# Performance work log

Measured on AMD Instinct MI355X. Metric: run time of the kernel, lower is better.

The kernel has to match this reference:

```python
import jax, jax.numpy as jnp
import numpy as np

N = 4096            # reservoir size
MAX_DIM = 4608      # max_dynamic_reservoir_dim
INPUT_DIM = 1024
LEAK_RATE = 0.1
SPIKE_THRESHOLD = 0.5
T, B = 128, 128


def setup_inputs() -> dict:
    key = jax.random.key(0)
    k1, k2, k3, k4 = jax.random.split(key, 4)
    x = jax.random.normal(k1, (T, B, INPUT_DIM), dtype=jnp.float32)
    state0 = jnp.zeros((B, MAX_DIM), dtype=jnp.float32)
    # keras RandomNormal default stddev=0.05 for reservoir, 0.1 for input/gate
    W_res = 0.05 * jax.random.normal(k2, (N, N), dtype=jnp.float32)
    W_in = 0.1 * jax.random.normal(k3, (N, INPUT_DIM), dtype=jnp.float32)
    W_gate = 0.1 * jax.random.normal(k4, (3 * N, INPUT_DIM), dtype=jnp.float32)
    return {"x": x, "state0": state0, "W_res": W_res, "W_in": W_in, "W_gate": W_gate}


def _cell(prev_padded, x_t, W_res, W_in, W_gate):
    prev = prev_padded[:, :N]                                  # [B, N]
    input_part = x_t @ W_in.T                                  # [B, N]
    reservoir_part = prev @ W_res                              # [B, N]
    gate = jax.nn.sigmoid(x_t @ W_gate.T)                      # [B, 3N]
    i_gate, f_gate, o_gate = jnp.split(gate, 3, axis=-1)
    state = (1.0 - LEAK_RATE) * (f_gate * prev) \
            + LEAK_RATE * jnp.tanh(i_gate * (input_part + reservoir_part))
    state = o_gate * state
    state = jnp.where(state > SPIKE_THRESHOLD, state - SPIKE_THRESHOLD, state)
    padded = jnp.concatenate(
        [state, jnp.zeros((state.shape[0], MAX_DIM - N), dtype=state.dtype)], axis=1)
    return padded


def reference(x, state0, W_res, W_in, W_gate):
    def step(carry, x_t):
        new = _cell(carry, x_t, W_res, W_in, W_gate)
        return new, new
    _, outs = jax.lax.scan(step, state0, x)   # outs: [T, B, MAX_DIM]
    return outs
```

## Files before the change

### kernel.cpp

```cpp
#include <hip/hip_runtime.h>
#include <hip/hip_bf16.h>
#include <hip/hip_fp16.h>

#define N_RES   4096
#define MAXD    4608
#define IN_DIM  1024
#define T_STEPS 128
#define B_SZ    128

typedef __attribute__((ext_vector_type(8))) short bf16x8;
typedef __attribute__((ext_vector_type(8))) _Float16 f16x8;
typedef __attribute__((ext_vector_type(4))) float f32x4;

__device__ __forceinline__ short f2bf(float x) {
  union { float f; unsigned u; } v; v.f = x;
  unsigned r = v.u + 0x7fffu + ((v.u >> 16) & 1u);
  return (short)(r >> 16);
}
__device__ __forceinline__ short f2h(float x) {
  union { _Float16 h; short s; } u; u.h = (_Float16)x; return u.s;
}
__device__ __forceinline__ float h2f(short s) {
  union { _Float16 h; short s; } u; u.s = s; return (float)u.h;
}

__device__ __forceinline__ void gload16(const void* g, void* l) {
  __builtin_amdgcn_global_load_lds(
      (const __attribute__((address_space(1))) void*)g,
      (__attribute__((address_space(3))) void*)l,
      16, 0, 0);
}

__global__ void k_zero_pad(float* __restrict__ out) {
  int row = blockIdx.x;
  int t = threadIdx.x;
  *(float4*)(out + (size_t)row * MAXD + N_RES + t * 4) = float4{0.f, 0.f, 0.f, 0.f};
}

__global__ void k_init_state(const float* __restrict__ s0,
                             float* __restrict__ sF, short* __restrict__ sB) {
  int i = blockIdx.x * 256 + threadIdx.x;
  int m = i >> 12, n = i & 4095;
  float v = s0[m * MAXD + n];
  sF[i] = v;
  sB[i] = f2bf(v);
}

__global__ void k_wres_t(const float* __restrict__ W, short* __restrict__ bt) {
  __shared__ float tile[64][65];
  int k0 = blockIdx.y * 64, n0 = blockIdx.x * 64;
  int tx = threadIdx.x & 63, ty = threadIdx.x >> 6;
  #pragma unroll
  for (int r = 0; r < 64; r += 4)
    tile[r + ty][tx] = W[(long)(k0 + r + ty) * N_RES + n0 + tx];
  __syncthreads();
  #pragma unroll
  for (int r = 0; r < 64; r += 4)
    bt[(long)(n0 + r + ty) * N_RES + k0 + tx] = f2bf(tile[tx][r + ty]);
}

__global__ void k_build_b2(const float* __restrict__ Win,
                           const float* __restrict__ Wg, short* __restrict__ B2) {
  int r = blockIdx.x;
  const float* src = (r < N_RES) ? (Win + (long)r * IN_DIM)
                                 : (Wg + (long)(r - N_RES) * IN_DIM);
  short* dst = B2 + (long)r * IN_DIM;
  for (int c = threadIdx.x; c < IN_DIM; c += 256)
    dst[c] = f2h(src[c]);
}

__global__ void k_build_a2(const float* __restrict__ x, short* __restrict__ A2, int t0) {
  int r = blockIdx.x;
  const float* src = x + (long)(t0 * B_SZ + r) * IN_DIM;
  short* dst = A2 + (long)r * IN_DIM;
  for (int c = threadIdx.x; c < IN_DIM; c += 256)
    dst[c] = f2h(src[c]);
}

__global__ __launch_bounds__(512, 2) void k_gemm_pre(
    const short* __restrict__ A2, const short* __restrict__ B2,
    _Float16* __restrict__ ip, _Float16* __restrict__ gates, int Mrows) {
  __shared__ short lA[2][2][128 * 64];
  __shared__ short lB[2][2][128 * 64];
  int tid = threadIdx.x, lane = tid & 63, wid = tid >> 6;
  int wr = wid >> 2, wc = wid & 3;

  int nwg = gridDim.x, orig = blockIdx.x;
  int mtiles = nwg >> 6;
  int mt, nt;
  if ((mtiles & 3) == 0) {
    int xcd = orig & 7, idx = orig >> 3;
    int w = idx & 31, sq = idx >> 5;
    nt = xcd * 8 + (w & 7);
    mt = sq * 4 + (w >> 3);
  } else {
    int qx = nwg >> 3, rx = nwg & 7, xcd = orig & 7;
    int wgid = (xcd < rx ? xcd * (qx + 1) : rx * (qx + 1) + (xcd - rx) * qx) + (orig >> 3);
    mt = wgid >> 6; nt = wgid & 63;
  }
  long m0 = (long)mt * 256, n0 = (long)nt * 256;
  long mclamp = Mrows - 1;

  int c0 = tid, c1 = 512 + tid;
  int r0 = c0 >> 3, r1 = c1 >> 3;
  int cc0 = ((c0 & 7) ^ (r0 & 7)) * 8, cc1 = ((c1 & 7) ^ (r1 & 7)) * 8;

  const short *pA00, *pA01, *pA10, *pA11, *pB00, *pB01, *pB10, *pB11;
  {
    long a00 = m0 + r0;       if (a00 > mclamp) a00 = mclamp;
    long a01 = m0 + r1;       if (a01 > mclamp) a01 = mclamp;
    long a10 = m0 + 128 + r0; if (a10 > mclamp) a10 = mclamp;
    long a11 = m0 + 128 + r1; if (a11 > mclamp) a11 = mclamp;
    pA00 = A2 + a00 * IN_DIM + cc0;  pA01 = A2 + a01 * IN_DIM + cc1;
    pA10 = A2 + a10 * IN_DIM + cc0;  pA11 = A2 + a11 * IN_DIM + cc1;
    pB00 = B2 + (n0 + r0) * IN_DIM + cc0;        pB01 = B2 + (n0 + r1) * IN_DIM + cc1;
    pB10 = B2 + (n0 + 128 + r0) * IN_DIM + cc0;  pB11 = B2 + (n0 + 128 + r1) * IN_DIM + cc1;
  }

  #define STG_A0(kt, b) { gload16(pA00 + (kt)*64, &lA[b][0][c0*8]); gload16(pA01 + (kt)*64, &lA[b][0][c1*8]); }
  #define STG_A1(kt, b) { gload16(pA10 + (kt)*64, &lA[b][1][c0*8]); gload16(pA11 + (kt)*64, &lA[b][1][c1*8]); }
  #define STG_B0(kt, b) { gload16(pB00 + (kt)*64, &lB[b][0][c0*8]); gload16(pB01 + (kt)*64, &lB[b][0][c1*8]); }
  #define STG_B1(kt, b) { gload16(pB10 + (kt)*64, &lB[b][1][c0*8]); gload16(pB11 + (kt)*64, &lB[b][1][c1*8]); }

  int lm = lane & 15;
  int colS0 = ((lane >> 4) * 8) ^ ((lane & 7) << 3);
  int colS1 = (32 + (lane >> 4) * 8) ^ ((lane & 7) << 3);
  int arow[4], brow[2];
  #pragma unroll
  for (int i = 0; i < 4; ++i) arow[i] = (wr * 64 + i * 16 + lm) * 64;
  #pragma unroll
  for (int j = 0; j < 2; ++j) brow[j] = (wc * 32 + j * 16 + lm) * 64;

  f16x8 aF[4][2], bFh[2][2][2];
  f32x4 acc[2][4][4] = {};

  #define RD_A(qm, b) { _Pragma("unroll") for (int i = 0; i < 4; ++i) {        \
      aF[i][0] = *(const f16x8*)&lA[b][qm][arow[i] + colS0];                   \
      aF[i][1] = *(const f16x8*)&lA[b][qm][arow[i] + colS1]; } }
  #define RD_B(h, b) { _Pragma("unroll") for (int j = 0; j < 2; ++j) {         \
      bFh[h][j][0] = *(const f16x8*)&lB[b][h][brow[j] + colS0];                \
      bFh[h][j][1] = *(const f16x8*)&lB[b][h][brow[j] + colS1]; } }
  #define MM(qm, qn) { __builtin_amdgcn_s_setprio(1);                          \
      _Pragma("unroll") for (int i = 0; i < 4; ++i)                            \
      _Pragma("unroll") for (int j = 0; j < 2; ++j) {                          \
        acc[qm][i][(qn)*2+j] = __builtin_amdgcn_mfma_f32_16x16x32_f16(         \
            aF[i][0], bFh[qn][j][0], acc[qm][i][(qn)*2+j], 0, 0, 0);           \
        acc[qm][i][(qn)*2+j] = __builtin_amdgcn_mfma_f32_16x16x32_f16(         \
            aF[i][1], bFh[qn][j][1], acc[qm][i][(qn)*2+j], 0, 0, 0); }         \
      __builtin_amdgcn_s_setprio(0); }

  STG_A0(0, 0); STG_B0(0, 0); STG_B1(0, 0); STG_A1(0, 0);

  const int nk = IN_DIM / 64;
  for (int kt = 0; kt < nk; ++kt) {
    int buf = kt & 1, nbuf = buf ^ 1;
    int ktn = (kt + 1 < nk) ? kt + 1 : kt;
    asm volatile("s_waitcnt vmcnt(4)\n\ts_barrier" ::: "memory");
    RD_A(0, buf); RD_B(0, buf);
    STG_A0(ktn, nbuf);
    MM(0, 0);
    asm volatile("s_barrier" ::: "memory");
    asm volatile("s_waitcnt vmcnt(4)\n\ts_barrier" ::: "memory");
    RD_B(1, buf);
    STG_B0(ktn, nbuf);
    MM(0, 1);
    asm volatile("s_barrier" ::: "memory");
    asm volatile("s_waitcnt vmcnt(4)\n\ts_barrier" ::: "memory");
    RD_A(1, buf);
    STG_B1(ktn, nbuf);
    MM(1, 0);
    asm volatile("s_barrier" ::: "memory");
    STG_A1(ktn, nbuf);
    MM(1, 1);
    asm volatile("s_barrier" ::: "memory");
  }
  #undef STG_A0
  #undef STG_A1
  #undef STG_B0
  #undef STG_B1
  #undef RD_A
  #undef RD_B
  #undef MM

  #pragma unroll
  for (int qm = 0; qm < 2; ++qm)
    #pragma unroll
    for (int i = 0; i < 4; ++i)
      #pragma unroll
      for (int qn = 0; qn < 2; ++qn)
        #pragma unroll
        for (int j = 0; j < 2; ++j)
          #pragma unroll
          for (int q = 0; q < 4; ++q) {
            long m = m0 + qm * 128 + wr * 64 + i * 16 + (lane >> 4) * 4 + q;
            long n = n0 + qn * 128 + wc * 32 + j * 16 + lm;
            if (m >= Mrows) continue;
            float v = acc[qm][i][qn * 2 + j][q];
            if (n < N_RES) {
              ip[m * N_RES + n] = (_Float16)v;
            } else {
              gates[m * 12288 + (n - N_RES)] = (_Float16)(1.f / (1.f + __expf(-v)));
            }
          }
}

__global__ __launch_bounds__(512) void k_step_gemm(
    const short* __restrict__ Abf,
    const short* __restrict__ Bt,
    float* __restrict__ part) {
  __shared__ short lA[3][64 * 128];
  __shared__ short lB[3][128 * 128];
  int tid = threadIdx.x, lane = tid & 63, wid = tid >> 6;
  int wm = wid >> 2, wn = wid & 3;

  int b = blockIdx.x;
  int xcd = b & 7, i2 = b >> 3;
  int m_h = i2 & 1, kc = (i2 >> 1) & 3, n_tl = i2 >> 3;
  int n_t = xcd * 4 + n_tl;
  int m0 = m_h * 64, n0 = n_t * 128, kb = kc * 1024;

  const short* pA[2];
  const short* pB[4];
  #pragma unroll
  for (int i = 0; i < 2; ++i) {
    int c = i * 512 + tid, row = c >> 4;
    pA[i] = Abf + (size_t)(m0 + row) * N_RES + kb + (((c & 15) ^ (row & 7)) * 8);
  }
  #pragma unroll
  for (int i = 0; i < 4; ++i) {
    int c = i * 512 + tid, row = c >> 4;
    pB[i] = Bt + (size_t)(n0 + row) * N_RES + kb + (((c & 15) ^ (row & 7)) * 8);
  }

  #define STAGE(kt, bi) { int k0s = (kt) * 128;                                \
    _Pragma("unroll") for (int i = 0; i < 2; ++i)                              \
      gload16(pA[i] + k0s, &lA[bi][(i * 512 + tid) * 8]);                      \
    _Pragma("unroll") for (int i = 0; i < 4; ++i)                              \
      gload16(pB[i] + k0s, &lB[bi][(i * 512 + tid) * 8]); }

  f32x4 acc[2][2] = {};

  #define COMPUTE(bi)                                                          \
    { _Pragma("unroll")                                                        \
      for (int kk = 0; kk < 128; kk += 32) {                                   \
        int colS = (kk + (lane >> 4) * 8) ^ ((lane & 7) << 3);                 \
        bf16x8 aF0 = *(const bf16x8*)&lA[bi][(wm * 32 + (lane & 15)) * 128 + colS];      \
        bf16x8 aF1 = *(const bf16x8*)&lA[bi][(wm * 32 + 16 + (lane & 15)) * 128 + colS]; \
        bf16x8 bF0 = *(const bf16x8*)&lB[bi][(wn * 32 + (lane & 15)) * 128 + colS];      \
        bf16x8 bF1 = *(const bf16x8*)&lB[bi][(wn * 32 + 16 + (lane & 15)) * 128 + colS]; \
        acc[0][0] = __builtin_amdgcn_mfma_f32_16x16x32_bf16(aF0, bF0, acc[0][0], 0, 0, 0); \
        acc[0][1] = __builtin_amdgcn_mfma_f32_16x16x32_bf16(aF0, bF1, acc[0][1], 0, 0, 0); \
        acc[1][0] = __builtin_amdgcn_mfma_f32_16x16x32_bf16(aF1, bF0, acc[1][0], 0, 0, 0); \
        acc[1][1] = __builtin_amdgcn_mfma_f32_16x16x32_bf16(aF1, bF1, acc[1][1], 0, 0, 0); \
      } }

  STAGE(0, 0);
  STAGE(1, 1);

  int bi = 0, sb = 2;
  for (int kt = 0; kt < 7; ++kt) {
    asm volatile("s_waitcnt vmcnt(6)" ::: "memory");
    __builtin_amdgcn_s_barrier();
    if (kt < 6) STAGE(kt + 2, sb);
    COMPUTE(bi);
    ++bi; if (bi == 3) bi = 0;
    ++sb; if (sb == 3) sb = 0;
  }
  asm volatile("s_waitcnt vmcnt(0)" ::: "memory");
  __builtin_amdgcn_s_barrier();
  COMPUTE(bi);
  #undef STAGE
  #undef COMPUTE

  float* dst = part + (size_t)kc * (B_SZ * N_RES);
  #pragma unroll
  for (int i = 0; i < 2; ++i)
    #pragma unroll
    for (int j = 0; j < 2; ++j)
      #pragma unroll
      for (int q = 0; q < 4; ++q) {
        int m = m0 + wm * 32 + i * 16 + (lane >> 4) * 4 + q;
        int n = n0 + wn * 32 + j * 16 + (lane & 15);
        dst[(size_t)m * N_RES + n] = acc[i][j][q];
      }
}

__global__ void k_step_red(
    const float* __restrict__ part,
    const _Float16* __restrict__ ip,
    const _Float16* __restrict__ gt,
    float* __restrict__ sF,
    short* __restrict__ sBw,
    float* __restrict__ out) {
  int e = (blockIdx.x * 256 + threadIdx.x) * 4;
  int m = e >> 12, n = e & 4095;
  float4 p0 = *(const float4*)(part + e);
  float4 p1 = *(const float4*)(part + (1 << 19) + e);
  float4 p2 = *(const float4*)(part + (2 << 19) + e);
  float4 p3 = *(const float4*)(part + (3 << 19) + e);
  short4 ipr = *(const short4*)((const short*)ip + e);
  const short* g = (const short*)gt + (size_t)m * 12288 + n;
  short4 igr = *(const short4*)g;
  short4 fgr = *(const short4*)(g + 4096);
  short4 ogr = *(const short4*)(g + 8192);
  float4 pr = *(const float4*)(sF + e);

  float res[4] = { p0.x + p1.x + p2.x + p3.x, p0.y + p1.y + p2.y + p3.y,
                   p0.z + p1.z + p2.z + p3.z, p0.w + p1.w + p2.w + p3.w };
  float prv[4] = { pr.x, pr.y, pr.z, pr.w };
  short ipa[4] = { ipr.x, ipr.y, ipr.z, ipr.w };
  short iga[4] = { igr.x, igr.y, igr.z, igr.w };
  short fga[4] = { fgr.x, fgr.y, fgr.z, fgr.w };
  short oga[4] = { ogr.x, ogr.y, ogr.z, ogr.w };

  float so[4];
  short sb[4];
  #pragma unroll
  for (int q = 0; q < 4; ++q) {
    float s = 0.9f * (h2f(fga[q]) * prv[q])
            + 0.1f * tanhf(h2f(iga[q]) * (h2f(ipa[q]) + res[q]));
    s = h2f(oga[q]) * s;
    if (s > 0.5f) s -= 0.5f;
    so[q] = s;
    sb[q] = f2bf(s);
  }
  *(float4*)(out + (size_t)m * MAXD + n) = float4{so[0], so[1], so[2], so[3]};
  *(float4*)(sF + e) = float4{so[0], so[1], so[2], so[3]};
  *(short4*)(sBw + e) = short4{sb[0], sb[1], sb[2], sb[3]};
}

extern "C" void kernel_launch(void* const* d_in, const int* in_sizes, int n_in,
                              void* d_out, int out_size, void* d_ws, size_t ws_size,
                              hipStream_t stream) {
  const float* x      = (const float*)d_in[0];
  const float* state0 = (const float*)d_in[1];
  const float* W_res  = (const float*)d_in[2];
  const float* W_in   = (const float*)d_in[3];
  const float* W_gate = (const float*)d_in[4];
  float* out = (float*)d_out;
  char* ws = (char*)d_ws;

  size_t off = 0;
  short* WresBT = (short*)(ws + off); off += (size_t)N_RES * N_RES * 2;
  short* B2     = (short*)(ws + off); off += (size_t)16384 * IN_DIM * 2;
  float* sF     = (float*)(ws + off); off += (size_t)B_SZ * N_RES * 4;
  short* sB0    = (short*)(ws + off); off += (size_t)B_SZ * N_RES * 2;
  short* sB1    = (short*)(ws + off); off += (size_t)B_SZ * N_RES * 2;
  float* part   = (float*)(ws + off); off += (size_t)4 * B_SZ * N_RES * 4;
  size_t fixed = off;
  size_t per = (size_t)B_SZ * IN_DIM * 2 + (size_t)B_SZ * N_RES * 2 + (size_t)B_SZ * 12288 * 2;

  int Tc = T_STEPS;
  while (Tc > 1 && fixed + (size_t)Tc * per > ws_size) Tc >>= 1;

  short*     A2  = (short*)(ws + fixed);
  _Float16*  ipb = (_Float16*)(ws + fixed + (size_t)Tc * B_SZ * IN_DIM * 2);
  _Float16*  gtb = (_Float16*)(ws + fixed + (size_t)Tc * B_SZ * IN_DIM * 2
                               + (size_t)Tc * B_SZ * N_RES * 2);

  k_zero_pad<<<T_STEPS * B_SZ, 128, 0, stream>>>(out);
  k_init_state<<<(B_SZ * N_RES) / 256, 256, 0, stream>>>(state0, sF, sB0);
  k_wres_t<<<dim3(64, 64), 256, 0, stream>>>(W_res, WresBT);
  k_build_b2<<<16384, 256, 0, stream>>>(W_in, W_gate, B2);

  for (int t0 = 0; t0 < T_STEPS; t0 += Tc) {
    k_build_a2<<<Tc * B_SZ, 256, 0, stream>>>(x, A2, t0);
    int Mrows = Tc * B_SZ;
    int mtiles = (Mrows + 255) / 256;
    k_gemm_pre<<<mtiles * 64, 512, 0, stream>>>(A2, B2, ipb, gtb, Mrows);
    for (int tl = 0; tl < Tc; ++tl) {
      int t = t0 + tl;
      const short* Ar = (t & 1) ? sB1 : sB0;
      short*       Aw = (t & 1) ? sB0 : sB1;
      k_step_gemm<<<256, 512, 0, stream>>>(Ar, WresBT, part);
      k_step_red<<<512, 256, 0, stream>>>(
          part,
          ipb + (size_t)tl * B_SZ * N_RES,
          gtb + (size_t)tl * B_SZ * 12288,
          sF, Aw,
          out + (size_t)t * B_SZ * MAXD);
    }
  }
}
```

Before: 2.795 ms.

## Retile recurrent step GEMM to full-M tiles with 8-way split-K; quantize gates to uint8

```diff
diff --git a/kernel.cpp b/kernel.cpp
--- a/kernel.cpp
+++ b/kernel.cpp
@@ -79,7 +79,7 @@
 
 __global__ __launch_bounds__(512, 2) void k_gemm_pre(
     const short* __restrict__ A2, const short* __restrict__ B2,
-    _Float16* __restrict__ ip, _Float16* __restrict__ gates, int Mrows) {
+    _Float16* __restrict__ ip, unsigned char* __restrict__ gates, int Mrows) {
   __shared__ short lA[2][2][128 * 64];
   __shared__ short lB[2][2][128 * 64];
   int tid = threadIdx.x, lane = tid & 63, wid = tid >> 6;
@@ -199,7 +199,8 @@
             if (n < N_RES) {
               ip[m * N_RES + n] = (_Float16)v;
             } else {
-              gates[m * 12288 + (n - N_RES)] = (_Float16)(1.f / (1.f + __expf(-v)));
+              float g = 1.f / (1.f + __expf(-v));
+              gates[m * 12288 + (n - N_RES)] = (unsigned char)(g * 255.f + 0.5f);
             }
           }
 }
@@ -208,50 +209,47 @@
     const short* __restrict__ Abf,
     const short* __restrict__ Bt,
     float* __restrict__ part) {
-  __shared__ short lA[3][64 * 128];
-  __shared__ short lB[3][128 * 128];
+  __shared__ short lA[3][128 * 64];
+  __shared__ short lB[3][128 * 64];
   int tid = threadIdx.x, lane = tid & 63, wid = tid >> 6;
   int wm = wid >> 2, wn = wid & 3;
 
   int b = blockIdx.x;
-  int xcd = b & 7, i2 = b >> 3;
-  int m_h = i2 & 1, kc = (i2 >> 1) & 3, n_tl = i2 >> 3;
-  int n_t = xcd * 4 + n_tl;
-  int m0 = m_h * 64, n0 = n_t * 128, kb = kc * 1024;
+  int xcd = b & 7, idx = b >> 3;
+  int n_t = xcd * 4 + (idx & 3);
+  int kc = idx >> 2;
+  int n0 = n_t * 128, kb = kc * 512;
 
   const short* pA[2];
-  const short* pB[4];
+  const short* pB[2];
   #pragma unroll
   for (int i = 0; i < 2; ++i) {
-    int c = i * 512 + tid, row = c >> 4;
-    pA[i] = Abf + (size_t)(m0 + row) * N_RES + kb + (((c & 15) ^ (row & 7)) * 8);
-  }
-  #pragma unroll
-  for (int i = 0; i < 4; ++i) {
-    int c = i * 512 + tid, row = c >> 4;
-    pB[i] = Bt + (size_t)(n0 + row) * N_RES + kb + (((c & 15) ^ (row & 7)) * 8);
-  }
-
-  #define STAGE(kt, bi) { int k0s = (kt) * 128;                                \
-    _Pragma("unroll") for (int i = 0; i < 2; ++i)                              \
-      gload16(pA[i] + k0s, &lA[bi][(i * 512 + tid) * 8]);                      \
-    _Pragma("unroll") for (int i = 0; i < 4; ++i)                              \
-      gload16(pB[i] + k0s, &lB[bi][(i * 512 + tid) * 8]); }
-
-  f32x4 acc[2][2] = {};
+    int c = i * 512 + tid, row = c >> 3;
+    int cc = ((c & 7) ^ (row & 7)) * 8;
+    pA[i] = Abf + (size_t)row * N_RES + kb + cc;
+    pB[i] = Bt + (size_t)(n0 + row) * N_RES + kb + cc;
+  }
+
+  #define STAGE(kt, bi) { int k0s = (kt) * 64;                                 \
+    gload16(pA[0] + k0s, &lA[bi][tid * 8]);                                    \
+    gload16(pA[1] + k0s, &lA[bi][(512 + tid) * 8]);                            \
+    gload16(pB[0] + k0s, &lB[bi][tid * 8]);                                    \
+    gload16(pB[1] + k0s, &lB[bi][(512 + tid) * 8]); }
+
+  f32x4 acc[4][2] = {};
 
   #define COMPUTE(bi)                                                          \
     { _Pragma("unroll")                                                        \
-      for (int kk = 0; kk < 128; kk += 32) {                                   \
+      for (int kk = 0; kk < 64; kk += 32) {                                    \
         int colS = (kk + (lane >> 4) * 8) ^ ((lane & 7) << 3);                 \
-        bf16x8 aF0 = *(const bf16x8*)&lA[bi][(wm * 32 + (lane & 15)) * 128 + colS];      \
-        bf16x8 aF1 = *(const bf16x8*)&lA[bi][(wm * 32 + 16 + (lane & 15)) * 128 + colS]; \
-        bf16x8 bF0 = *(const bf16x8*)&lB[bi][(wn * 32 + (lane & 15)) * 128 + colS];      \
-        bf16x8 bF1 = *(const bf16x8*)&lB[bi][(wn * 32 + 16 + (lane & 15)) * 128 + colS]; \
-        acc[0][0] = __builtin_amdgcn_mfma_f32_16x16x32_bf16(aF0, bF0, acc[0][0], 0, 0, 0); \
-        acc[0][1] = __builtin_amdgcn_mfma_f32_16x16x32_bf16(aF0, bF1, acc[0][1], 0, 0, 0); \
-        acc[1][0] = __builtin_amdgcn_mfma_f32_16x16x32_bf16(aF1, bF0, acc[1][0], 0, 0, 0); \
-        acc[1][1] = __builtin_amdgcn_mfma_f32_16x16x32_bf16(aF1, bF1, acc[1][1], 0, 0, 0); \
+        bf16x8 aF[4], bF[2];                                                   \
+        _Pragma("unroll") for (int i = 0; i < 4; ++i)                          \
+          aF[i] = *(const bf16x8*)&lA[bi][(wm * 64 + i * 16 + (lane & 15)) * 64 + colS]; \
+        _Pragma("unroll") for (int j = 0; j < 2; ++j)                          \
+          bF[j] = *(const bf16x8*)&lB[bi][(wn * 32 + j * 16 + (lane & 15)) * 64 + colS]; \
+        _Pragma("unroll") for (int i = 0; i < 4; ++i)                          \
+        _Pragma("unroll") for (int j = 0; j < 2; ++j)                          \
+          acc[i][j] = __builtin_amdgcn_mfma_f32_16x16x32_bf16(aF[i], bF[j], acc[i][j], 0, 0, 0); \
       } }
 
   STAGE(0, 0);
@@ -259,7 +257,7 @@
 
   int bi = 0, sb = 2;
   for (int kt = 0; kt < 7; ++kt) {
-    asm volatile("s_waitcnt vmcnt(6)" ::: "memory");
+    asm volatile("s_waitcnt vmcnt(4)" ::: "memory");
     __builtin_amdgcn_s_barrier();
     if (kt < 6) STAGE(kt + 2, sb);
     COMPUTE(bi);
@@ -274,12 +272,12 @@
 
   float* dst = part + (size_t)kc * (B_SZ * N_RES);
   #pragma unroll
-  for (int i = 0; i < 2; ++i)
+  for (int i = 0; i < 4; ++i)
     #pragma unroll
     for (int j = 0; j < 2; ++j)
       #pragma unroll
       for (int q = 0; q < 4; ++q) {
-        int m = m0 + wm * 32 + i * 16 + (lane >> 4) * 4 + q;
+        int m = wm * 64 + i * 16 + (lane >> 4) * 4 + q;
         int n = n0 + wn * 32 + j * 16 + (lane & 15);
         dst[(size_t)m * N_RES + n] = acc[i][j][q];
       }
@@ -288,38 +286,39 @@
 __global__ void k_step_red(
     const float* __restrict__ part,
     const _Float16* __restrict__ ip,
-    const _Float16* __restrict__ gt,
+    const unsigned char* __restrict__ gt,
     float* __restrict__ sF,
     short* __restrict__ sBw,
     float* __restrict__ out) {
   int e = (blockIdx.x * 256 + threadIdx.x) * 4;
   int m = e >> 12, n = e & 4095;
-  float4 p0 = *(const float4*)(part + e);
-  float4 p1 = *(const float4*)(part + (1 << 19) + e);
-  float4 p2 = *(const float4*)(part + (2 << 19) + e);
-  float4 p3 = *(const float4*)(part + (3 << 19) + e);
+  float res[4] = {0.f, 0.f, 0.f, 0.f};
+  #pragma unroll
+  for (int k = 0; k < 8; ++k) {
+    float4 p = *(const float4*)(part + ((size_t)k << 19) + e);
+    res[0] += p.x; res[1] += p.y; res[2] += p.z; res[3] += p.w;
+  }
   short4 ipr = *(const short4*)((const short*)ip + e);
-  const short* g = (const short*)gt + (size_t)m * 12288 + n;
-  short4 igr = *(const short4*)g;
-  short4 fgr = *(const short4*)(g + 4096);
-  short4 ogr = *(const short4*)(g + 8192);
+  const unsigned char* g = gt + (size_t)m * 12288 + n;
+  uchar4 igr = *(const uchar4*)g;
+  uchar4 fgr = *(const uchar4*)(g + 4096);
+  uchar4 ogr = *(const uchar4*)(g + 8192);
   float4 pr = *(const float4*)(sF + e);
 
-  float res[4] = { p0.x + p1.x + p2.x + p3.x, p0.y + p1.y + p2.y + p3.y,
-                   p0.z + p1.z + p2.z + p3.z, p0.w + p1.w + p2.w + p3.w };
   float prv[4] = { pr.x, pr.y, pr.z, pr.w };
   short ipa[4] = { ipr.x, ipr.y, ipr.z, ipr.w };
-  short iga[4] = { igr.x, igr.y, igr.z, igr.w };
-  short fga[4] = { fgr.x, fgr.y, fgr.z, fgr.w };
-  short oga[4] = { ogr.x, ogr.y, ogr.z, ogr.w };
-
+  unsigned char iga[4] = { igr.x, igr.y, igr.z, igr.w };
+  unsigned char fga[4] = { fgr.x, fgr.y, fgr.z, fgr.w };
+  unsigned char oga[4] = { ogr.x, ogr.y, ogr.z, ogr.w };
+
+  const float is = 1.f / 255.f;
   float so[4];
   short sb[4];
   #pragma unroll
   for (int q = 0; q < 4; ++q) {
-    float s = 0.9f * (h2f(fga[q]) * prv[q])
-            + 0.1f * tanhf(h2f(iga[q]) * (h2f(ipa[q]) + res[q]));
-    s = h2f(oga[q]) * s;
+    float s = 0.9f * ((float)fga[q] * is * prv[q])
+            + 0.1f * tanhf((float)iga[q] * is * (h2f(ipa[q]) + res[q]));
+    s = (float)oga[q] * is * s;
     if (s > 0.5f) s -= 0.5f;
     so[q] = s;
     sb[q] = f2bf(s);
@@ -346,17 +345,17 @@
   float* sF     = (float*)(ws + off); off += (size_t)B_SZ * N_RES * 4;
   short* sB0    = (short*)(ws + off); off += (size_t)B_SZ * N_RES * 2;
   short* sB1    = (short*)(ws + off); off += (size_t)B_SZ * N_RES * 2;
-  float* part   = (float*)(ws + off); off += (size_t)4 * B_SZ * N_RES * 4;
+  float* part   = (float*)(ws + off); off += (size_t)8 * B_SZ * N_RES * 4;
   size_t fixed = off;
-  size_t per = (size_t)B_SZ * IN_DIM * 2 + (size_t)B_SZ * N_RES * 2 + (size_t)B_SZ * 12288 * 2;
+  size_t per = (size_t)B_SZ * IN_DIM * 2 + (size_t)B_SZ * N_RES * 2 + (size_t)B_SZ * 12288;
 
   int Tc = T_STEPS;
   while (Tc > 1 && fixed + (size_t)Tc * per > ws_size) Tc >>= 1;
 
-  short*     A2  = (short*)(ws + fixed);
-  _Float16*  ipb = (_Float16*)(ws + fixed + (size_t)Tc * B_SZ * IN_DIM * 2);
-  _Float16*  gtb = (_Float16*)(ws + fixed + (size_t)Tc * B_SZ * IN_DIM * 2
-                               + (size_t)Tc * B_SZ * N_RES * 2);
+  short*          A2  = (short*)(ws + fixed);
+  _Float16*       ipb = (_Float16*)(ws + fixed + (size_t)Tc * B_SZ * IN_DIM * 2);
+  unsigned char*  gtb = (unsigned char*)(ws + fixed + (size_t)Tc * B_SZ * IN_DIM * 2
+                                         + (size_t)Tc * B_SZ * N_RES * 2);
 
   k_zero_pad<<<T_STEPS * B_SZ, 128, 0, stream>>>(out);
   k_init_state<<<(B_SZ * N_RES) / 256, 256, 0, stream>>>(state0, sF, sB0);
```

Result: slower. 3.130 ms (+12.0%).
